# Optimization experiments

Hardware: AMD Instinct MI355X
Metric: run time of the kernel (lower is better)

The kernel has to match this reference:

```python
import jax, jax.numpy as jnp
import numpy as np

N = 50000   # nodes
E = 800000  # edges
IN = 256    # input feature dim
H = 4       # heads (per layer)
D = 64      # num_hidden per head
C = 16      # n_clusters
NEG = 0.2   # leaky_relu negative slope


def _gat_conv(x, W, attn_l, attn_r, src, dst):
    """DGL GATConv (no residual, no dropout at eval), activation=elu.
    x: [N, F_in], W: [F_in, H*D], attn_l/attn_r: [H, D]. Returns [N, H, D]."""
    feat = (x @ W).reshape(N, H, D)                      # [N,H,D]
    el = jnp.sum(feat * attn_l, axis=-1)                 # [N,H]
    er = jnp.sum(feat * attn_r, axis=-1)                 # [N,H]
    e = jax.nn.leaky_relu(el[src] + er[dst], NEG)        # [E,H]
    # numerically stable segment softmax over incoming edges of each dst node
    emax = jax.ops.segment_max(e, dst, num_segments=N)   # [N,H]
    emax = jnp.where(jnp.isfinite(emax), emax, 0.0)
    ee = jnp.exp(e - emax[dst])                          # [E,H]
    denom = jax.ops.segment_sum(ee, dst, num_segments=N) # [N,H]
    a = ee / jnp.maximum(denom[dst], 1e-9)               # [E,H]
    msg = feat[src] * a[:, :, None]                      # [E,H,D]
    rst = jax.ops.segment_sum(msg, dst, num_segments=N)  # [N,H,D]
    return jax.nn.elu(rst)


def setup_inputs() -> dict:
    key = jax.random.key(0)
    ks = jax.random.split(key, 12)
    def w(k, shape, fan):
        return jax.random.normal(k, shape, jnp.float32) * np.float32(1.0 / np.sqrt(fan))
    return {
        "x": jax.random.normal(ks[0], (N, IN), jnp.float32),
        "src": jax.random.randint(ks[1], (E,), 0, N, jnp.int32),
        "dst": jax.random.randint(ks[2], (E,), 0, N, jnp.int32),
        "W0": w(ks[3], (IN, H * D), IN),
        "al0": w(ks[4], (H, D), D),
        "ar0": w(ks[5], (H, D), D),
        "W1": w(ks[6], (H * D, H * D), H * D),
        "al1": w(ks[7], (H, D), D),
        "ar1": w(ks[8], (H, D), D),
        "Wc": w(ks[9], (D, C), D),
        "bc": jnp.zeros((C,), jnp.float32),
    }


def reference(x, src, dst, W0, al0, ar0, W1, al1, ar1, Wc, bc):
    h = _gat_conv(x, W0, al0, ar0, src, dst)              # [N,H,D]
    h = _gat_conv(h.reshape(N, H * D), W1, al1, ar1, src, dst)
    heads = jnp.transpose(h, (1, 0, 2))                   # [H,N,D]
    # original bug: same cluster layer (index num_layers-1) used for every head
    cs = jax.nn.softmax(jnp.einsum("hnd,dc->hnc", heads, Wc) + bc, axis=-1)  # [H,N,C]
    # pack (heads, cs) into one array along last dim for a single output
    return jnp.concatenate([heads, cs], axis=-1)          # [H,N,D+C]
```

## Files before the change

### kernel.cpp

```cpp
#include <hip/hip_runtime.h>
#include <hip/hip_bf16.h>
#include <math.h>

#define N_NODES 50000
#define N_EDGES 800000
#define NH 4
#define ND 64
#define NF 256
#define NC 16
#define NEG_SLOPE 0.2f
#define NSLICE 8
#define SLICE_W 32

typedef __attribute__((ext_vector_type(8))) short bf16x8;
typedef __attribute__((ext_vector_type(4))) float f32x4;

__device__ __forceinline__ float elu_f(float x) {
    return x > 0.f ? x : (__expf(x) - 1.f);
}

__device__ __forceinline__ ushort bf16_rne(float f) {
    union { float f; unsigned u; } v; v.f = f;
    unsigned u = v.u;
    u += 0x7fffu + ((u >> 16) & 1u);
    return (ushort)(u >> 16);
}

__device__ __forceinline__ float bf2f(ushort u) {
    return __uint_as_float(((unsigned)u) << 16);
}

__global__ __launch_bounds__(256) void cast_bf16_kernel(const float* __restrict__ in,
                                                        ushort* __restrict__ out, int n8) {
    int i = blockIdx.x * 256 + threadIdx.x;
    if (i >= n8) return;
    float4 a = *(const float4*)(in + i * 8);
    float4 b = *(const float4*)(in + i * 8 + 4);
    ushort o[8] = {bf16_rne(a.x), bf16_rne(a.y), bf16_rne(a.z), bf16_rne(a.w),
                   bf16_rne(b.x), bf16_rne(b.y), bf16_rne(b.z), bf16_rne(b.w)};
    *(bf16x8*)(out + i * 8) = *(bf16x8*)o;
}

__global__ __launch_bounds__(256) void castWt_kernel(const float* __restrict__ W0,
                                                     const float* __restrict__ W1,
                                                     ushort* __restrict__ Wt0,
                                                     ushort* __restrict__ Wt1) {
    const float* W = (blockIdx.x < 256) ? W0 : W1;
    ushort* Wt = (blockIdx.x < 256) ? Wt0 : Wt1;
    int n = blockIdx.x & 255;
    int k = threadIdx.x;
    Wt[n * 256 + k] = bf16_rne(W[k * 256 + n]);
}

__global__ __launch_bounds__(256) void gemm_bf16(const ushort* __restrict__ A,
                                                 const ushort* __restrict__ Bt,
                                                 ushort* __restrict__ Cs,
                                                 const float* __restrict__ al,
                                                 const float* __restrict__ ar,
                                                 float* __restrict__ el,
                                                 float* __restrict__ er, int M) {
    __shared__ __align__(16) ushort As[128 * 64];
    __shared__ __align__(16) ushort Bs[128 * 64];
    const int t = threadIdx.x;
    const int l = t & 63;
    const int w = t >> 6;
    const int wm = (w >> 1) * 64, wn = (w & 1) * 64;
    const int m0 = blockIdx.x * 128, n0 = blockIdx.y * 128;
    const int lr = l & 15, lk = l >> 4;

    f32x4 acc[4][4] = {};
    const int sr = t >> 3;
    const int sc = t & 7;
    const int scw = sc ^ (sr & 7);

    for (int k0 = 0; k0 < 256; k0 += 64) {
        #pragma unroll
        for (int q = 0; q < 4; ++q) {
            int row = q * 32 + sr;
            int ga = min(m0 + row, M - 1);
            bf16x8 va = *(const bf16x8*)(A + (size_t)ga * 256 + k0 + sc * 8);
            *(bf16x8*)(&As[row * 64 + scw * 8]) = va;
            bf16x8 vb = *(const bf16x8*)(Bt + (size_t)(n0 + row) * 256 + k0 + sc * 8);
            *(bf16x8*)(&Bs[row * 64 + scw * 8]) = vb;
        }
        __syncthreads();
        #pragma unroll
        for (int kk = 0; kk < 2; ++kk) {
            bf16x8 af[4], bfr[4];
            #pragma unroll
            for (int mi = 0; mi < 4; ++mi) {
                int row = wm + mi * 16 + lr;
                int kb = kk * 4 + lk;
                af[mi] = *(const bf16x8*)(&As[row * 64 + (kb ^ (row & 7)) * 8]);
            }
            #pragma unroll
            for (int ni = 0; ni < 4; ++ni) {
                int col = wn + ni * 16 + lr;
                int kb = kk * 4 + lk;
                bfr[ni] = *(const bf16x8*)(&Bs[col * 64 + (kb ^ (col & 7)) * 8]);
            }
            #pragma unroll
            for (int mi = 0; mi < 4; ++mi)
                #pragma unroll
                for (int ni = 0; ni < 4; ++ni)
                    acc[mi][ni] = __builtin_amdgcn_mfma_f32_16x16x32_bf16(af[mi], bfr[ni], acc[mi][ni], 0, 0, 0);
        }
        __syncthreads();
    }
    const int h = (n0 + wn) >> 6;
    float alv[4], arv[4];
    #pragma unroll
    for (int ni = 0; ni < 4; ++ni) {
        alv[ni] = al[h * ND + ni * 16 + lr];
        arv[ni] = ar[h * ND + ni * 16 + lr];
    }
    #pragma unroll
    for (int mi = 0; mi < 4; ++mi) {
        #pragma unroll
        for (int j = 0; j < 4; ++j) {
            int row = m0 + wm + mi * 16 + lk * 4 + j;
            float pe = 0.f, pr = 0.f;
            #pragma unroll
            for (int ni = 0; ni < 4; ++ni) {
                int col = n0 + wn + ni * 16 + lr;
                float v = acc[mi][ni][j];
                pe += v * alv[ni];
                pr += v * arv[ni];
                if (row < M)
                    Cs[(size_t)(col >> 5) * N_NODES * SLICE_W + (size_t)row * SLICE_W + (col & 31)] = bf16_rne(v);
            }
            #pragma unroll
            for (int m = 1; m <= 8; m <<= 1) {
                pe += __shfl_xor(pe, m, 64);
                pr += __shfl_xor(pr, m, 64);
            }
            if (lr == 0 && row < M) {
                el[h * N_NODES + row] = pe;
                er[h * N_NODES + row] = pr;
            }
        }
    }
}

__global__ __launch_bounds__(256) void hist_kernel(const int* __restrict__ dst, int* __restrict__ count) {
    int e = blockIdx.x * 256 + threadIdx.x;
    if (e < N_EDGES) atomicAdd(&count[dst[e]], 1);
}

__global__ __launch_bounds__(256) void scan1_kernel(const int* __restrict__ counts,
                                                    int* __restrict__ offs,
                                                    int* __restrict__ bsums) {
    __shared__ int sh[256];
    int tid = threadIdx.x;
    int i = blockIdx.x * 256 + tid;
    int v = (i < N_NODES) ? counts[i] : 0;
    sh[tid] = v;
    __syncthreads();
    #pragma unroll
    for (int ofs = 1; ofs < 256; ofs <<= 1) {
        int t = (tid >= ofs) ? sh[tid - ofs] : 0;
        __syncthreads();
        sh[tid] += t;
        __syncthreads();
    }
    if (i < N_NODES) offs[i] = sh[tid] - v;
    if (tid == 255) bsums[blockIdx.x] = sh[255];
}

__global__ __launch_bounds__(256) void scan2_kernel(const int* __restrict__ bsums,
                                                    int* __restrict__ boffs, int nb) {
    __shared__ int sh[256];
    int tid = threadIdx.x;
    int v = (tid < nb) ? bsums[tid] : 0;
    sh[tid] = v;
    __syncthreads();
    #pragma unroll
    for (int ofs = 1; ofs < 256; ofs <<= 1) {
        int t = (tid >= ofs) ? sh[tid - ofs] : 0;
        __syncthreads();
        sh[tid] += t;
        __syncthreads();
    }
    if (tid < nb) boffs[tid] = sh[tid] - v;
}

__global__ __launch_bounds__(256) void scan3_kernel(int* __restrict__ offs,
                                                    const int* __restrict__ boffs,
                                                    int* __restrict__ cursor) {
    int i = blockIdx.x * 256 + threadIdx.x;
    if (i < N_NODES) {
        int v = offs[i] + boffs[i >> 8];
        offs[i] = v;
        cursor[i] = v;
    }
    if (i == 0) offs[N_NODES] = N_EDGES;
}

__global__ __launch_bounds__(256) void scatter_kernel(const int* __restrict__ src,
                                                      const int* __restrict__ dst,
                                                      int* __restrict__ cursor,
                                                      int* __restrict__ csrc) {
    int e = blockIdx.x * 256 + threadIdx.x;
    if (e >= N_EDGES) return;
    int p = atomicAdd(&cursor[dst[e]], 1);
    csrc[p] = src[e];
}

#define AGG5_EDGE(K)                                                                \
        int i##K = s0 + min(t + K, degc);                                           \
        int a##K = csrc[i##K];
#define AGG5_EL(K)                                                                  \
        float e##K = elh[a##K];
#define AGG5_Q(K)                                                                   \
        ushort4 q##K = *(const ushort4*)(base + a##K * SLICE_W + fc * 4);
#define AGG5_W(K)                                                                   \
        float x##K = e##K + ern; x##K = fmaxf(x##K, NEG_SLOPE * x##K);              \
        float w##K = (t + K < deg) ? __expf(x##K) : 0.f;
#define AGG5_ACC(K)                                                                 \
        acc.x += w##K * bf2f(q##K.x);                                               \
        acc.y += w##K * bf2f(q##K.y);                                               \
        acc.z += w##K * bf2f(q##K.z);                                               \
        acc.w += w##K * bf2f(q##K.w);                                               \
        dsum += w##K;

#define AGG5_BODY()                                                                 \
    int b = blockIdx.x;                                                             \
    int slice = b & 7;                                                              \
    int wid = threadIdx.x >> 6;                                                     \
    int lane = threadIdx.x & 63;                                                    \
    int nn = lane >> 3;                                                             \
    int fc = lane & 7;                                                              \
    int h = slice >> 1;                                                             \
    int n = (b >> 3) * 32 + wid * 8 + nn;                                           \
    int nc = min(n, N_NODES - 1);                                                   \
    const ushort* base = fs + (size_t)slice * (N_NODES * SLICE_W);                  \
    const float* elh = el + (size_t)h * N_NODES;                                    \
    int s0 = offs[nc];                                                              \
    int deg = (n < N_NODES) ? (offs[nc + 1] - s0) : 0;                              \
    int degc = max(deg - 1, 0);                                                     \
    float ern = er[(size_t)h * N_NODES + nc];                                       \
    int md = deg;                                                                   \
    md = max(md, __shfl_xor(md, 8, 64));                                            \
    md = max(md, __shfl_xor(md, 16, 64));                                           \
    md = max(md, __shfl_xor(md, 32, 64));                                           \
    float4 acc = make_float4(0.f, 0.f, 0.f, 0.f);                                   \
    float dsum = 0.f;                                                               \
    for (int t = 0; t < md; t += 8) {                                               \
        AGG5_EDGE(0) AGG5_EDGE(1) AGG5_EDGE(2) AGG5_EDGE(3)                         \
        AGG5_EDGE(4) AGG5_EDGE(5) AGG5_EDGE(6) AGG5_EDGE(7)                         \
        AGG5_EL(0) AGG5_EL(1) AGG5_EL(2) AGG5_EL(3)                                 \
        AGG5_EL(4) AGG5_EL(5) AGG5_EL(6) AGG5_EL(7)                                 \
        AGG5_Q(0) AGG5_Q(1) AGG5_Q(2) AGG5_Q(3)                                     \
        AGG5_Q(4) AGG5_Q(5) AGG5_Q(6) AGG5_Q(7)                                     \
        AGG5_W(0) AGG5_W(1) AGG5_W(2) AGG5_W(3)                                     \
        AGG5_W(4) AGG5_W(5) AGG5_W(6) AGG5_W(7)                                     \
        AGG5_ACC(0) AGG5_ACC(1) AGG5_ACC(2) AGG5_ACC(3)                             \
        AGG5_ACC(4) AGG5_ACC(5) AGG5_ACC(6) AGG5_ACC(7)                             \
    }                                                                               \
    float inv = 1.f / fmaxf(dsum, 1e-9f);

__global__ __launch_bounds__(256) void agg5_l0(const ushort* __restrict__ fs,
                                               const int* __restrict__ csrc,
                                               const int* __restrict__ offs,
                                               const float* __restrict__ el,
                                               const float* __restrict__ er,
                                               ushort* __restrict__ hbuf) {
    AGG5_BODY()
    if (n < N_NODES) {
        ushort o[4] = {bf16_rne(elu_f(acc.x * inv)), bf16_rne(elu_f(acc.y * inv)),
                       bf16_rne(elu_f(acc.z * inv)), bf16_rne(elu_f(acc.w * inv))};
        *(ushort4*)(hbuf + (size_t)n * NF + slice * SLICE_W + fc * 4) = *(ushort4*)o;
    }
}

__global__ __launch_bounds__(256) void agg5_final(const ushort* __restrict__ fs,
                                                  const int* __restrict__ csrc,
                                                  const int* __restrict__ offs,
                                                  const float* __restrict__ el,
                                                  const float* __restrict__ er,
                                                  float* __restrict__ out) {
    AGG5_BODY()
    if (n < N_NODES) {
        float4 v = make_float4(elu_f(acc.x * inv), elu_f(acc.y * inv),
                               elu_f(acc.z * inv), elu_f(acc.w * inv));
        size_t p = (size_t)h * N_NODES * (ND + NC) + (size_t)n * (ND + NC)
                 + (slice & 1) * SLICE_W + fc * 4;
        *(float4*)(out + p) = v;
    }
}

__global__ __launch_bounds__(256) void cluster_kernel(const float* __restrict__ Wc,
                                                      const float* __restrict__ bc,
                                                      float* __restrict__ out) {
    __shared__ float WcS[ND * NC];
    __shared__ float bcS[NC];
    int tid = threadIdx.x;
    #pragma unroll
    for (int i = 0; i < 4; ++i) WcS[i * 256 + tid] = Wc[i * 256 + tid];
    if (tid < NC) bcS[tid] = bc[tid];
    __syncthreads();
    int wid = tid >> 6;
    int lane = tid & 63;
    int h = lane >> 4, c = lane & 15;
    int n = blockIdx.x * 4 + wid;
    size_t base = (size_t)h * N_NODES * (ND + NC) + (size_t)n * (ND + NC);
    const float* hp = out + base;
    float acc = bcS[c];
    #pragma unroll
    for (int dd = 0; dd < 16; ++dd) {
        float4 f4 = *(const float4*)(hp + dd * 4);
        acc += f4.x * WcS[(dd * 4 + 0) * NC + c];
        acc += f4.y * WcS[(dd * 4 + 1) * NC + c];
        acc += f4.z * WcS[(dd * 4 + 2) * NC + c];
        acc += f4.w * WcS[(dd * 4 + 3) * NC + c];
    }
    float m = acc;
    m = fmaxf(m, __shfl_xor(m, 1, 64));
    m = fmaxf(m, __shfl_xor(m, 2, 64));
    m = fmaxf(m, __shfl_xor(m, 4, 64));
    m = fmaxf(m, __shfl_xor(m, 8, 64));
    float e = __expf(acc - m);
    float s = e;
    s += __shfl_xor(s, 1, 64);
    s += __shfl_xor(s, 2, 64);
    s += __shfl_xor(s, 4, 64);
    s += __shfl_xor(s, 8, 64);
    out[base + ND + c] = e / s;
}

extern "C" void kernel_launch(void* const* d_in, const int* in_sizes, int n_in,
                              void* d_out, int out_size, void* d_ws, size_t ws_size,
                              hipStream_t stream) {
    const float* x   = (const float*)d_in[0];
    const int* src   = (const int*)d_in[1];
    const int* dst   = (const int*)d_in[2];
    const float* W0  = (const float*)d_in[3];
    const float* al0 = (const float*)d_in[4];
    const float* ar0 = (const float*)d_in[5];
    const float* W1  = (const float*)d_in[6];
    const float* al1 = (const float*)d_in[7];
    const float* ar1 = (const float*)d_in[8];
    const float* Wc  = (const float*)d_in[9];
    const float* bc  = (const float*)d_in[10];
    float* out = (float*)d_out;

    char* ws = (char*)d_ws;
    size_t off = 0;
    auto alloc = [&](size_t bytes) { void* p = ws + off; off = (off + bytes + 255) & ~(size_t)255; return p; };
    ushort* featsl = (ushort*)alloc((size_t)N_NODES * NF * 2);
    ushort* xbf    = (ushort*)alloc((size_t)N_NODES * NF * 2);
    ushort* hbuf   = (ushort*)alloc((size_t)N_NODES * NF * 2);
    ushort* Wt0    = (ushort*)alloc((size_t)256 * 256 * 2);
    ushort* Wt1    = (ushort*)alloc((size_t)256 * 256 * 2);
    float*  el     = (float*)alloc((size_t)N_NODES * NH * 4);
    float*  er     = (float*)alloc((size_t)N_NODES * NH * 4);
    int* counts    = (int*)alloc((size_t)N_NODES * 4);
    int* offs      = (int*)alloc((size_t)(N_NODES + 1) * 4);
    int* cursor    = (int*)alloc((size_t)N_NODES * 4);
    int* csrc      = (int*)alloc((size_t)N_EDGES * 4);
    int* bsums     = (int*)alloc(256 * 4);
    int* boffs     = (int*)alloc(256 * 4);

    const int EB = (N_EDGES + 255) / 256;
    const int NB = (N_NODES + 255) / 256;
    const int GEMM_MB = (N_NODES + 127) / 128;
    const int C8 = (N_NODES * NF / 8 + 255) / 256;
    const int AGG_B = NSLICE * ((N_NODES + 31) / 32);

    hipMemsetAsync(counts, 0, (size_t)N_NODES * 4, stream);
    hist_kernel<<<EB, 256, 0, stream>>>(dst, counts);
    scan1_kernel<<<NB, 256, 0, stream>>>(counts, offs, bsums);
    scan2_kernel<<<1, 256, 0, stream>>>(bsums, boffs, NB);
    scan3_kernel<<<NB, 256, 0, stream>>>(offs, boffs, cursor);
    scatter_kernel<<<EB, 256, 0, stream>>>(src, dst, cursor, csrc);

    castWt_kernel<<<512, 256, 0, stream>>>(W0, W1, Wt0, Wt1);
    cast_bf16_kernel<<<C8, 256, 0, stream>>>(x, xbf, N_NODES * NF / 8);

    gemm_bf16<<<dim3(GEMM_MB, 2), 256, 0, stream>>>(xbf, Wt0, featsl, al0, ar0, el, er, N_NODES);
    agg5_l0<<<AGG_B, 256, 0, stream>>>(featsl, csrc, offs, el, er, hbuf);

    gemm_bf16<<<dim3(GEMM_MB, 2), 256, 0, stream>>>(hbuf, Wt1, featsl, al1, ar1, el, er, N_NODES);
    agg5_final<<<AGG_B, 256, 0, stream>>>(featsl, csrc, offs, el, er, out);

    cluster_kernel<<<N_NODES / 4, 256, 0, stream>>>(Wc, bc, out);
}
```

Measured before the change: 363.6 us.

## Sort nodes by degree and share edge weights across lanes via swizzle

Adds a counting sort of destination nodes by in-degree (histogram, scan, scatter) so each wave processes nodes of similar degree, reducing divergence from the per-wave max-degree loop. Within the aggregation loop, each of the 8 feature lanes of a node now computes the attention weight for one edge and broadcasts index and weight to the others with ds_swizzle, replacing eight redundant el loads and exps per lane. The softmax denominator becomes a cross-lane reduction. This adds three small preprocessing kernels plus a memset, and output writes become scattered through the permutation.

New measurement: 625.2 us. 1.72x slower.

```diff
diff --git a/kernel.cpp b/kernel.cpp
--- a/kernel.cpp
+++ b/kernel.cpp
@@ -206,85 +206,113 @@
     csrc[p] = src[e];
 }
 
-#define AGG5_EDGE(K)                                                                \
-        int i##K = s0 + min(t + K, degc);                                           \
-        int a##K = csrc[i##K];
-#define AGG5_EL(K)                                                                  \
-        float e##K = elh[a##K];
-#define AGG5_Q(K)                                                                   \
-        ushort4 q##K = *(const ushort4*)(base + a##K * SLICE_W + fc * 4);
-#define AGG5_W(K)                                                                   \
-        float x##K = e##K + ern; x##K = fmaxf(x##K, NEG_SLOPE * x##K);              \
-        float w##K = (t + K < deg) ? __expf(x##K) : 0.f;
-#define AGG5_ACC(K)                                                                 \
+__global__ __launch_bounds__(256) void deg_hist_kernel(const int* __restrict__ counts,
+                                                       int* __restrict__ dcnt) {
+    int i = blockIdx.x * 256 + threadIdx.x;
+    if (i < N_NODES) atomicAdd(&dcnt[min(counts[i], 63)], 1);
+}
+
+__global__ __launch_bounds__(64) void deg_scan_kernel(const int* __restrict__ dcnt,
+                                                      int* __restrict__ dcur) {
+    if (threadIdx.x == 0) {
+        int s = 0;
+        for (int d = 0; d < 64; ++d) { int c = dcnt[d]; dcur[d] = s; s += c; }
+    }
+}
+
+__global__ __launch_bounds__(256) void deg_scatter_kernel(const int* __restrict__ counts,
+                                                          const int* __restrict__ offs,
+                                                          int* __restrict__ dcur,
+                                                          int* __restrict__ nperm,
+                                                          int2* __restrict__ sinfo) {
+    int i = blockIdx.x * 256 + threadIdx.x;
+    if (i >= N_NODES) return;
+    int d = counts[i];
+    int pos = atomicAdd(&dcur[min(d, 63)], 1);
+    nperm[pos] = i;
+    sinfo[pos] = make_int2(offs[i], d);
+}
+
+#define AGG6_E(K)                                                                   \
+        int a##K = __builtin_amdgcn_ds_swizzle(a_own, 0x18 | (K << 5));             \
+        float w##K = __uint_as_float((unsigned)__builtin_amdgcn_ds_swizzle(         \
+                         (int)__float_as_uint(w_own), 0x18 | (K << 5)));            \
+        ushort4 q##K = *(const ushort4*)(base + a##K * SLICE_W + fc4);              \
         acc.x += w##K * bf2f(q##K.x);                                               \
         acc.y += w##K * bf2f(q##K.y);                                               \
         acc.z += w##K * bf2f(q##K.z);                                               \
-        acc.w += w##K * bf2f(q##K.w);                                               \
-        dsum += w##K;
-
-#define AGG5_BODY()                                                                 \
+        acc.w += w##K * bf2f(q##K.w);
+
+#define AGG6_BODY()                                                                 \
     int b = blockIdx.x;                                                             \
     int slice = b & 7;                                                              \
     int wid = threadIdx.x >> 6;                                                     \
     int lane = threadIdx.x & 63;                                                    \
     int nn = lane >> 3;                                                             \
     int fc = lane & 7;                                                              \
+    int fc4 = fc * 4;                                                               \
     int h = slice >> 1;                                                             \
-    int n = (b >> 3) * 32 + wid * 8 + nn;                                           \
-    int nc = min(n, N_NODES - 1);                                                   \
+    int pos = (b >> 3) * 32 + wid * 8 + nn;                                         \
+    int cpos = min(pos, N_NODES - 1);                                               \
+    int n = nperm[cpos];                                                            \
+    int2 si = sinfo[cpos];                                                          \
+    int s0 = si.x;                                                                  \
+    int deg = (pos < N_NODES) ? si.y : 0;                                           \
+    int degc = max(deg - 1, 0);                                                     \
     const ushort* base = fs + (size_t)slice * (N_NODES * SLICE_W);                  \
     const float* elh = el + (size_t)h * N_NODES;                                    \
-    int s0 = offs[nc];                                                              \
-    int deg = (n < N_NODES) ? (offs[nc + 1] - s0) : 0;                              \
-    int degc = max(deg - 1, 0);                                                     \
-    float ern = er[(size_t)h * N_NODES + nc];                                       \
+    float ern = er[(size_t)h * N_NODES + n];                                        \
     int md = deg;                                                                   \
     md = max(md, __shfl_xor(md, 8, 64));                                            \
     md = max(md, __shfl_xor(md, 16, 64));                                           \
     md = max(md, __shfl_xor(md, 32, 64));                                           \
     float4 acc = make_float4(0.f, 0.f, 0.f, 0.f);                                   \
-    float dsum = 0.f;                                                               \
-    for (int t = 0; t < md; t += 8) {                                               \
-        AGG5_EDGE(0) AGG5_EDGE(1) AGG5_EDGE(2) AGG5_EDGE(3)                         \
-        AGG5_EDGE(4) AGG5_EDGE(5) AGG5_EDGE(6) AGG5_EDGE(7)                         \
-        AGG5_EL(0) AGG5_EL(1) AGG5_EL(2) AGG5_EL(3)                                 \
-        AGG5_EL(4) AGG5_EL(5) AGG5_EL(6) AGG5_EL(7)                                 \
-        AGG5_Q(0) AGG5_Q(1) AGG5_Q(2) AGG5_Q(3)                                     \
-        AGG5_Q(4) AGG5_Q(5) AGG5_Q(6) AGG5_Q(7)                                     \
-        AGG5_W(0) AGG5_W(1) AGG5_W(2) AGG5_W(3)                                     \
-        AGG5_W(4) AGG5_W(5) AGG5_W(6) AGG5_W(7)                                     \
-        AGG5_ACC(0) AGG5_ACC(1) AGG5_ACC(2) AGG5_ACC(3)                             \
-        AGG5_ACC(4) AGG5_ACC(5) AGG5_ACC(6) AGG5_ACC(7)                             \
+    float wsum = 0.f;                                                               \
+    int tf = fc;                                                                    \
+    for (int t = 0; t < md; t += 8, tf += 8) {                                      \
+        int idx = s0 + min(tf, degc);                                               \
+        int a_own = csrc[idx];                                                      \
+        float e_own = elh[a_own];                                                   \
+        float x = e_own + ern;                                                      \
+        x = fmaxf(x, NEG_SLOPE * x);                                                \
+        float w_own = (tf < deg) ? __expf(x) : 0.f;                                 \
+        wsum += w_own;                                                              \
+        AGG6_E(0) AGG6_E(1) AGG6_E(2) AGG6_E(3)                                     \
+        AGG6_E(4) AGG6_E(5) AGG6_E(6) AGG6_E(7)                                     \
     }                                                                               \
-    float inv = 1.f / fmaxf(dsum, 1e-9f);
-
-__global__ __launch_bounds__(256) void agg5_l0(const ushort* __restrict__ fs,
+    wsum += __shfl_xor(wsum, 1, 64);                                                \
+    wsum += __shfl_xor(wsum, 2, 64);                                                \
+    wsum += __shfl_xor(wsum, 4, 64);                                                \
+    float inv = 1.f / fmaxf(wsum, 1e-9f);
+
+__global__ __launch_bounds__(256) void agg6_l0(const ushort* __restrict__ fs,
                                                const int* __restrict__ csrc,
-                                               const int* __restrict__ offs,
+                                               const int* __restrict__ nperm,
+                                               const int2* __restrict__ sinfo,
                                                const float* __restrict__ el,
                                                const float* __restrict__ er,
                                                ushort* __restrict__ hbuf) {
-    AGG5_BODY()
-    if (n < N_NODES) {
+    AGG6_BODY()
+    if (pos < N_NODES) {
         ushort o[4] = {bf16_rne(elu_f(acc.x * inv)), bf16_rne(elu_f(acc.y * inv)),
                        bf16_rne(elu_f(acc.z * inv)), bf16_rne(elu_f(acc.w * inv))};
-        *(ushort4*)(hbuf + (size_t)n * NF + slice * SLICE_W + fc * 4) = *(ushort4*)o;
-    }
-}
-
-__global__ __launch_bounds__(256) void agg5_final(const ushort* __restrict__ fs,
+        *(ushort4*)(hbuf + (size_t)n * NF + slice * SLICE_W + fc4) = *(ushort4*)o;
+    }
+}
+
+__global__ __launch_bounds__(256) void agg6_final(const ushort* __restrict__ fs,
                                                   const int* __restrict__ csrc,
-                                                  const int* __restrict__ offs,
+                                                  const int* __restrict__ nperm,
+                                                  const int2* __restrict__ sinfo,
                                                   const float* __restrict__ el,
                                                   const float* __restrict__ er,
                                                   float* __restrict__ out) {
-    AGG5_BODY()
-    if (n < N_NODES) {
+    AGG6_BODY()
+    if (pos < N_NODES) {
         float4 v = make_float4(elu_f(acc.x * inv), elu_f(acc.y * inv),
                                elu_f(acc.z * inv), elu_f(acc.w * inv));
         size_t p = (size_t)h * N_NODES * (ND + NC) + (size_t)n * (ND + NC)
-                 + (slice & 1) * SLICE_W + fc * 4;
+                 + (slice & 1) * SLICE_W + fc4;
         *(float4*)(out + p) = v;
     }
 }
@@ -358,6 +386,10 @@
     int* offs      = (int*)alloc((size_t)(N_NODES + 1) * 4);
     int* cursor    = (int*)alloc((size_t)N_NODES * 4);
     int* csrc      = (int*)alloc((size_t)N_EDGES * 4);
+    int* nperm     = (int*)alloc((size_t)N_NODES * 4);
+    int2* sinfo    = (int2*)alloc((size_t)N_NODES * 8);
+    int* dcnt      = (int*)alloc(64 * 4);
+    int* dcur      = (int*)alloc(64 * 4);
     int* bsums     = (int*)alloc(256 * 4);
     int* boffs     = (int*)alloc(256 * 4);
 
@@ -374,14 +406,19 @@
     scan3_kernel<<<NB, 256, 0, stream>>>(offs, boffs, cursor);
     scatter_kernel<<<EB, 256, 0, stream>>>(src, dst, cursor, csrc);
 
+    hipMemsetAsync(dcnt, 0, 64 * 4, stream);
+    deg_hist_kernel<<<NB, 256, 0, stream>>>(counts, dcnt);
+    deg_scan_kernel<<<1, 64, 0, stream>>>(dcnt, dcur);
+    deg_scatter_kernel<<<NB, 256, 0, stream>>>(counts, offs, dcur, nperm, sinfo);
+
     castWt_kernel<<<512, 256, 0, stream>>>(W0, W1, Wt0, Wt1);
     cast_bf16_kernel<<<C8, 256, 0, stream>>>(x, xbf, N_NODES * NF / 8);
 
     gemm_bf16<<<dim3(GEMM_MB, 2), 256, 0, stream>>>(xbf, Wt0, featsl, al0, ar0, el, er, N_NODES);
-    agg5_l0<<<AGG_B, 256, 0, stream>>>(featsl, csrc, offs, el, er, hbuf);
+    agg6_l0<<<AGG_B, 256, 0, stream>>>(featsl, csrc, nperm, sinfo, el, er, hbuf);
 
     gemm_bf16<<<dim3(GEMM_MB, 2), 256, 0, stream>>>(hbuf, Wt1, featsl, al1, ar1, el, er, N_NODES);
-    agg5_final<<<AGG_B, 256, 0, stream>>>(featsl, csrc, offs, el, er, out);
+    agg6_final<<<AGG_B, 256, 0, stream>>>(featsl, csrc, nperm, sinfo, el, er, out);
 
     cluster_kernel<<<N_NODES / 4, 256, 0, stream>>>(Wc, bc, out);
 }
```

## Precompute per-edge attention weights in padded CSR slots before aggregation

Applied to the files above, without the earlier changes.

Adds an edge-weight kernel that computes exp(leaky_relu(el[src]+er[dst])) once per CSR slot for all four heads and packs it with the source index as int2 per head. Each node's CSR segment is padded up to a multiple of 8 using sentinel slots, which the edge kernel turns into zero weights. el/er move to a node-major layout so one float4 load serves all heads. The aggregation inner loop then drops the el gather, the exp and the degree masking, in exchange for an extra kernel per layer, a memset, and writing and re-reading a sizable edge-weight buffer.

After: 379.9 us. 4.5% more time.

```diff
diff --git a/kernel.cpp b/kernel.cpp
--- a/kernel.cpp
+++ b/kernel.cpp
@@ -11,6 +11,7 @@
 #define NEG_SLOPE 0.2f
 #define NSLICE 8
 #define SLICE_W 32
+#define SLOT_CAP (N_EDGES + 8 * N_NODES)
 
 typedef __attribute__((ext_vector_type(8))) short bf16x8;
 typedef __attribute__((ext_vector_type(4))) float f32x4;
@@ -135,8 +136,8 @@
                 pr += __shfl_xor(pr, m, 64);
             }
             if (lr == 0 && row < M) {
-                el[h * N_NODES + row] = pe;
-                er[h * N_NODES + row] = pr;
+                el[row * 4 + h] = pe;
+                er[row * 4 + h] = pr;
             }
         }
     }
@@ -153,7 +154,7 @@
     __shared__ int sh[256];
     int tid = threadIdx.x;
     int i = blockIdx.x * 256 + tid;
-    int v = (i < N_NODES) ? counts[i] : 0;
+    int v = (i < N_NODES) ? ((counts[i] + 8) & ~7) : 0;
     sh[tid] = v;
     __syncthreads();
     #pragma unroll
@@ -186,44 +187,74 @@
 
 __global__ __launch_bounds__(256) void scan3_kernel(int* __restrict__ offs,
                                                     const int* __restrict__ boffs,
+                                                    const int* __restrict__ counts,
                                                     int* __restrict__ cursor) {
     int i = blockIdx.x * 256 + threadIdx.x;
     if (i < N_NODES) {
         int v = offs[i] + boffs[i >> 8];
         offs[i] = v;
         cursor[i] = v;
-    }
-    if (i == 0) offs[N_NODES] = N_EDGES;
+        if (i == N_NODES - 1) offs[N_NODES] = v + ((counts[i] + 8) & ~7);
+    }
 }
 
 __global__ __launch_bounds__(256) void scatter_kernel(const int* __restrict__ src,
                                                       const int* __restrict__ dst,
                                                       int* __restrict__ cursor,
-                                                      int* __restrict__ csrc) {
+                                                      int* __restrict__ csrc,
+                                                      int* __restrict__ cdst) {
     int e = blockIdx.x * 256 + threadIdx.x;
     if (e >= N_EDGES) return;
-    int p = atomicAdd(&cursor[dst[e]], 1);
+    int d = dst[e];
+    int p = atomicAdd(&cursor[d], 1);
     csrc[p] = src[e];
-}
-
-#define AGG5_EDGE(K)                                                                \
-        int i##K = s0 + min(t + K, degc);                                           \
-        int a##K = csrc[i##K];
-#define AGG5_EL(K)                                                                  \
-        float e##K = elh[a##K];
-#define AGG5_Q(K)                                                                   \
-        ushort4 q##K = *(const ushort4*)(base + a##K * SLICE_W + fc * 4);
-#define AGG5_W(K)                                                                   \
-        float x##K = e##K + ern; x##K = fmaxf(x##K, NEG_SLOPE * x##K);              \
-        float w##K = (t + K < deg) ? __expf(x##K) : 0.f;
-#define AGG5_ACC(K)                                                                 \
-        acc.x += w##K * bf2f(q##K.x);                                               \
-        acc.y += w##K * bf2f(q##K.y);                                               \
-        acc.z += w##K * bf2f(q##K.z);                                               \
-        acc.w += w##K * bf2f(q##K.w);                                               \
-        dsum += w##K;
-
-#define AGG5_BODY()                                                                 \
+    cdst[p] = d;
+}
+
+__global__ __launch_bounds__(256) void edge_w_kernel(const int* __restrict__ csrc,
+                                                     const int* __restrict__ cdst,
+                                                     const float* __restrict__ el,
+                                                     const float* __restrict__ er,
+                                                     int2* __restrict__ ew) {
+    int i = blockIdx.x * 256 + threadIdx.x;
+    if (i >= SLOT_CAP) return;
+    int s = csrc[i];
+    if (s < 0) {
+        int2 z = make_int2(0, 0);
+        #pragma unroll
+        for (int hh = 0; hh < 4; ++hh) ew[(size_t)hh * SLOT_CAP + i] = z;
+        return;
+    }
+    int d = cdst[i];
+    float4 lv = *(const float4*)(el + s * 4);
+    float4 rv = *(const float4*)(er + d * 4);
+    float lvv[4] = {lv.x, lv.y, lv.z, lv.w};
+    float rvv[4] = {rv.x, rv.y, rv.z, rv.w};
+    #pragma unroll
+    for (int hh = 0; hh < 4; ++hh) {
+        float v = lvv[hh] + rvv[hh];
+        v = v > 0.f ? v : NEG_SLOPE * v;
+        float o = __expf(v);
+        ew[(size_t)hh * SLOT_CAP + i] = make_int2(s, __float_as_int(o));
+    }
+}
+
+#define AGG7_E(K)                                                                   \
+        int idx##K = s0 + min(t + K, dlim);                                         \
+        int2 e##K = ewh[idx##K];
+#define AGG7_Q(K)                                                                   \
+        ushort4 q##K = *(const ushort4*)(basef + e##K.x * SLICE_W);
+#define AGG7_ACC(K)                                                                 \
+        {                                                                           \
+            float wv = __int_as_float(e##K.y);                                      \
+            acc.x += wv * bf2f(q##K.x);                                             \
+            acc.y += wv * bf2f(q##K.y);                                             \
+            acc.z += wv * bf2f(q##K.z);                                             \
+            acc.w += wv * bf2f(q##K.w);                                             \
+            dsum += wv;                                                             \
+        }
+
+#define AGG7_BODY()                                                                 \
     int b = blockIdx.x;                                                             \
     int slice = b & 7;                                                              \
     int wid = threadIdx.x >> 6;                                                     \
@@ -233,39 +264,32 @@
     int h = slice >> 1;                                                             \
     int n = (b >> 3) * 32 + wid * 8 + nn;                                           \
     int nc = min(n, N_NODES - 1);                                                   \
-    const ushort* base = fs + (size_t)slice * (N_NODES * SLICE_W);                  \
-    const float* elh = el + (size_t)h * N_NODES;                                    \
+    const ushort* basef = fs + (size_t)slice * (N_NODES * SLICE_W) + fc * 4;        \
+    const int2* ewh = ew + (size_t)h * SLOT_CAP;                                    \
     int s0 = offs[nc];                                                              \
-    int deg = (n < N_NODES) ? (offs[nc + 1] - s0) : 0;                              \
-    int degc = max(deg - 1, 0);                                                     \
-    float ern = er[(size_t)h * N_NODES + nc];                                       \
-    int md = deg;                                                                   \
+    int degp = (n < N_NODES) ? (offs[nc + 1] - s0) : 0;                             \
+    int dlim = max(degp - 1, 0);                                                    \
+    int md = degp;                                                                  \
     md = max(md, __shfl_xor(md, 8, 64));                                            \
     md = max(md, __shfl_xor(md, 16, 64));                                           \
     md = max(md, __shfl_xor(md, 32, 64));                                           \
     float4 acc = make_float4(0.f, 0.f, 0.f, 0.f);                                   \
     float dsum = 0.f;                                                               \
     for (int t = 0; t < md; t += 8) {                                               \
-        AGG5_EDGE(0) AGG5_EDGE(1) AGG5_EDGE(2) AGG5_EDGE(3)                         \
-        AGG5_EDGE(4) AGG5_EDGE(5) AGG5_EDGE(6) AGG5_EDGE(7)                         \
-        AGG5_EL(0) AGG5_EL(1) AGG5_EL(2) AGG5_EL(3)                                 \
-        AGG5_EL(4) AGG5_EL(5) AGG5_EL(6) AGG5_EL(7)                                 \
-        AGG5_Q(0) AGG5_Q(1) AGG5_Q(2) AGG5_Q(3)                                     \
-        AGG5_Q(4) AGG5_Q(5) AGG5_Q(6) AGG5_Q(7)                                     \
-        AGG5_W(0) AGG5_W(1) AGG5_W(2) AGG5_W(3)                                     \
-        AGG5_W(4) AGG5_W(5) AGG5_W(6) AGG5_W(7)                                     \
-        AGG5_ACC(0) AGG5_ACC(1) AGG5_ACC(2) AGG5_ACC(3)                             \
-        AGG5_ACC(4) AGG5_ACC(5) AGG5_ACC(6) AGG5_ACC(7)                             \
+        AGG7_E(0) AGG7_E(1) AGG7_E(2) AGG7_E(3)                                     \
+        AGG7_E(4) AGG7_E(5) AGG7_E(6) AGG7_E(7)                                     \
+        AGG7_Q(0) AGG7_Q(1) AGG7_Q(2) AGG7_Q(3)                                     \
+        AGG7_Q(4) AGG7_Q(5) AGG7_Q(6) AGG7_Q(7)                                     \
+        AGG7_ACC(0) AGG7_ACC(1) AGG7_ACC(2) AGG7_ACC(3)                             \
+        AGG7_ACC(4) AGG7_ACC(5) AGG7_ACC(6) AGG7_ACC(7)                             \
     }                                                                               \
     float inv = 1.f / fmaxf(dsum, 1e-9f);
 
-__global__ __launch_bounds__(256) void agg5_l0(const ushort* __restrict__ fs,
-                                               const int* __restrict__ csrc,
+__global__ __launch_bounds__(256) void agg7_l0(const ushort* __restrict__ fs,
                                                const int* __restrict__ offs,
-                                               const float* __restrict__ el,
-                                               const float* __restrict__ er,
+                                               const int2* __restrict__ ew,
                                                ushort* __restrict__ hbuf) {
-    AGG5_BODY()
+    AGG7_BODY()
     if (n < N_NODES) {
         ushort o[4] = {bf16_rne(elu_f(acc.x * inv)), bf16_rne(elu_f(acc.y * inv)),
                        bf16_rne(elu_f(acc.z * inv)), bf16_rne(elu_f(acc.w * inv))};
@@ -273,13 +297,11 @@
     }
 }
 
-__global__ __launch_bounds__(256) void agg5_final(const ushort* __restrict__ fs,
-                                                  const int* __restrict__ csrc,
+__global__ __launch_bounds__(256) void agg7_final(const ushort* __restrict__ fs,
                                                   const int* __restrict__ offs,
-                                                  const float* __restrict__ el,
-                                                  const float* __restrict__ er,
+                                                  const int2* __restrict__ ew,
                                                   float* __restrict__ out) {
-    AGG5_BODY()
+    AGG7_BODY()
     if (n < N_NODES) {
         float4 v = make_float4(elu_f(acc.x * inv), elu_f(acc.y * inv),
                                elu_f(acc.z * inv), elu_f(acc.w * inv));
@@ -354,15 +376,18 @@
     ushort* Wt1    = (ushort*)alloc((size_t)256 * 256 * 2);
     float*  el     = (float*)alloc((size_t)N_NODES * NH * 4);
     float*  er     = (float*)alloc((size_t)N_NODES * NH * 4);
+    int2*   ew     = (int2*)alloc((size_t)NH * SLOT_CAP * 8);
     int* counts    = (int*)alloc((size_t)N_NODES * 4);
     int* offs      = (int*)alloc((size_t)(N_NODES + 1) * 4);
     int* cursor    = (int*)alloc((size_t)N_NODES * 4);
-    int* csrc      = (int*)alloc((size_t)N_EDGES * 4);
+    int* csrc      = (int*)alloc((size_t)SLOT_CAP * 4);
+    int* cdst      = (int*)alloc((size_t)SLOT_CAP * 4);
     int* bsums     = (int*)alloc(256 * 4);
     int* boffs     = (int*)alloc(256 * 4);
 
     const int EB = (N_EDGES + 255) / 256;
     const int NB = (N_NODES + 255) / 256;
+    const int SB = (SLOT_CAP + 255) / 256;
     const int GEMM_MB = (N_NODES + 127) / 128;
     const int C8 = (N_NODES * NF / 8 + 255) / 256;
     const int AGG_B = NSLICE * ((N_NODES + 31) / 32);
@@ -371,17 +396,20 @@
     hist_kernel<<<EB, 256, 0, stream>>>(dst, counts);
     scan1_kernel<<<NB, 256, 0, stream>>>(counts, offs, bsums);
     scan2_kernel<<<1, 256, 0, stream>>>(bsums, boffs, NB);
-    scan3_kernel<<<NB, 256, 0, stream>>>(offs, boffs, cursor);
-    scatter_kernel<<<EB, 256, 0, stream>>>(src, dst, cursor, csrc);
+    scan3_kernel<<<NB, 256, 0, stream>>>(offs, boffs, counts, cursor);
+    hipMemsetAsync(csrc, 0xFF, (size_t)SLOT_CAP * 4, stream);
+    scatter_kernel<<<EB, 256, 0, stream>>>(src, dst, cursor, csrc, cdst);
 
     castWt_kernel<<<512, 256, 0, stream>>>(W0, W1, Wt0, Wt1);
     cast_bf16_kernel<<<C8, 256, 0, stream>>>(x, xbf, N_NODES * NF / 8);
 
     gemm_bf16<<<dim3(GEMM_MB, 2), 256, 0, stream>>>(xbf, Wt0, featsl, al0, ar0, el, er, N_NODES);
-    agg5_l0<<<AGG_B, 256, 0, stream>>>(featsl, csrc, offs, el, er, hbuf);
+    edge_w_kernel<<<SB, 256, 0, stream>>>(csrc, cdst, el, er, ew);
+    agg7_l0<<<AGG_B, 256, 0, stream>>>(featsl, offs, ew, hbuf);
 
     gemm_bf16<<<dim3(GEMM_MB, 2), 256, 0, stream>>>(hbuf, Wt1, featsl, al1, ar1, el, er, N_NODES);
-    agg5_final<<<AGG_B, 256, 0, stream>>>(featsl, csrc, offs, el, er, out);
+    edge_w_kernel<<<SB, 256, 0, stream>>>(csrc, cdst, el, er, ew);
+    agg7_final<<<AGG_B, 256, 0, stream>>>(featsl, offs, ew, out);
 
     cluster_kernel<<<N_NODES / 4, 256, 0, stream>>>(Wc, bc, out);
 }
```
